# Kernel tuning notes

Hardware: AMD Instinct MI355X
Metric: run time of the kernel (lower is better)

Reference implementation:

```python
import jax, jax.numpy as jnp
import numpy as np

N, E, DIN, DH, DP = 100000, 1600000, 128, 128, 64
BN_EPS = 1e-5


def setup_inputs() -> dict:
    key = jax.random.key(0)
    ks = jax.random.split(key, 24)

    def lin(k, fan_in, shape):
        return jax.random.normal(k, shape, jnp.float32) / np.sqrt(fan_in)

    inp = {
        "x": jax.random.normal(ks[0], (N, DIN), jnp.float32),
        "edge_index": jax.random.randint(ks[1], (2, E), 0, N, dtype=jnp.int32),
        "edge_type": jax.random.randint(ks[2], (E,), 0, 2, dtype=jnp.int32),
        "edge_weight": jax.random.uniform(ks[3], (E,), jnp.float32),
        "seed_node_id": 12345,
        # feature transform
        "ft_w": lin(ks[4], DIN, (DIN, DH)),
        "ft_b": jnp.zeros((DH,), jnp.float32),
        # GCN block 0: 2 layers, stacked along axis 0
        "g0_w": lin(ks[5], DH, (2, DH, DH)),
        "g0_b": jnp.zeros((2, DH), jnp.float32),
        "g0_gamma": jnp.ones((2, DH), jnp.float32),
        "g0_beta": jnp.zeros((2, DH), jnp.float32),
        "g0_rm": 0.1 * jax.random.normal(ks[6], (2, DH), jnp.float32),
        "g0_rv": 0.5 + jax.random.uniform(ks[7], (2, DH), jnp.float32),
        # GCN block 1
        "g1_w": lin(ks[8], DH, (2, DH, DH)),
        "g1_b": jnp.zeros((2, DH), jnp.float32),
        "g1_gamma": jnp.ones((2, DH), jnp.float32),
        "g1_beta": jnp.zeros((2, DH), jnp.float32),
        "g1_rm": 0.1 * jax.random.normal(ks[9], (2, DH), jnp.float32),
        "g1_rv": 0.5 + jax.random.uniform(ks[10], (2, DH), jnp.float32),
        # predictor (input = 4*DH)
        "p_w1": lin(ks[11], 4 * DH, (4 * DH, DP)),
        "p_b1": jnp.zeros((DP,), jnp.float32),
        "p_w2": lin(ks[12], DP, (DP, DP)),
        "p_b2": jnp.zeros((DP,), jnp.float32),
        "p_w3": lin(ks[13], DP, (DP, 1)),
        "p_b3": jnp.zeros((1,), jnp.float32),
    }
    return inp


def _gcn_conv(x, src, dst, w_e, W, b):
    # PyG GCNConv: linear transform, add self-loops (weight 1), symmetric norm, scatter-add, bias.
    h = x @ W                                               # [N, DH]
    deg = jax.ops.segment_sum(w_e, dst, num_segments=N) + 1.0
    dis = jax.lax.rsqrt(deg)
    coef = dis[src] * w_e * dis[dst]                        # [E]
    agg = jax.ops.segment_sum(coef[:, None] * h[src], dst, num_segments=N)
    return agg + h * (1.0 / deg)[:, None] + b               # self-loop norm = 1/deg


def _bn_eval(o, gamma, beta, rm, rv):
    return (o - rm) * gamma * jax.lax.rsqrt(rv + BN_EPS) + beta


def _gcn_block(x, src, dst, w_e, W, b, gamma, beta, rm, rv):
    # layer 0: no residual, followed by ReLU (dropout is a no-op in eval)
    h = _bn_eval(_gcn_conv(x, src, dst, w_e, W[0], b[0]), gamma[0], beta[0], rm[0], rv[0])
    h = jax.nn.relu(h)
    # layer 1: residual (in == out)
    h2 = _bn_eval(_gcn_conv(h, src, dst, w_e, W[1], b[1]), gamma[1], beta[1], rm[1], rv[1])
    return h2 + h


def reference(x, edge_index, edge_type, edge_weight, seed_node_id,
              ft_w, ft_b,
              g0_w, g0_b, g0_gamma, g0_beta, g0_rm, g0_rv,
              g1_w, g1_b, g1_gamma, g1_beta, g1_rm, g1_rv,
              p_w1, p_b1, p_w2, p_b2, p_w3, p_b3):
    src, dst = edge_index[0], edge_index[1]
    h = jax.nn.relu(x @ ft_w + ft_b)
    # edge-type masking via zeroed weights (identical math to slicing the edge list)
    w0 = edge_weight * (edge_type == 0).astype(edge_weight.dtype)
    w1 = edge_weight * (edge_type == 1).astype(edge_weight.dtype)
    x0 = _gcn_block(h, src, dst, w0, g0_w, g0_b, g0_gamma, g0_beta, g0_rm, g0_rv)
    x1 = _gcn_block(h, src, dst, w1, g1_w, g1_b, g1_gamma, g1_beta, g1_rm, g1_rv)
    s0 = jnp.broadcast_to(x0[seed_node_id], (N, DH))
    s1 = jnp.broadcast_to(x1[seed_node_id], (N, DH))
    xc = jnp.concatenate([x0, x1, s0, s1], axis=1)          # [N, 4*DH]
    z = jax.nn.relu(xc @ p_w1 + p_b1)
    z = jax.nn.relu(z @ p_w2 + p_b2)
    out = z @ p_w3 + p_b3                                   # [N, 1]
    return out.squeeze(-1)                                  # [N]
```

## Files before the change

### kernel.cpp

```cpp
#include <hip/hip_runtime.h>
#include <hip/hip_bf16.h>
#include <stdint.h>

#define N_NODES 100000

typedef unsigned short us16;
typedef short bf16x8 __attribute__((ext_vector_type(8)));
typedef float f32x4 __attribute__((ext_vector_type(4)));

__device__ __forceinline__ float us2f(us16 u){
  union{ unsigned int i; float f; } x; x.i = ((unsigned int)u) << 16; return x.f;
}
__device__ __forceinline__ us16 f2us(float f){
  union{ float f; unsigned int i; } x; x.f = f;
  unsigned int i = x.i;
  unsigned int r = (i + 0x7FFFu + ((i >> 16) & 1u)) >> 16;
  return (us16)r;
}

__global__ __launch_bounds__(256) void k_init(int* __restrict__ cnt, int n2){
  int i = blockIdx.x*256 + threadIdx.x;
  if (i < n2) cnt[i]=0;
}

__global__ __launch_bounds__(256) void k_cnt(const int* __restrict__ dst,
                                             const int* __restrict__ et,
                                             int* __restrict__ cnt,
                                             int* __restrict__ eofs, int E){
  int e = blockIdx.x*256 + threadIdx.x;
  if (e>=E) return;
  int d = dst[e]; int t = et[e];
  eofs[e] = atomicAdd(&cnt[t*N_NODES + d], 1);
}

__global__ __launch_bounds__(256) void k_scan_reduce(const int* __restrict__ in, int* __restrict__ bsum, int M){
  __shared__ int sd[256];
  int base = blockIdx.x*2048; int t = threadIdx.x;
  int sum = 0;
  #pragma unroll
  for(int i=0;i<8;i++){ int p = base + t*8 + i; if(p<M) sum += in[p]; }
  sd[t]=sum; __syncthreads();
  for(int s=128;s>0;s>>=1){ if(t<s) sd[t]+=sd[t+s]; __syncthreads(); }
  if(t==0) bsum[blockIdx.x]=sd[0];
}
__global__ void k_scan_top(int* __restrict__ bsum, int B){
  if (threadIdx.x==0){ int run=0; for(int i=0;i<B;i++){ int v=bsum[i]; bsum[i]=run; run+=v; } }
}
__global__ __launch_bounds__(256) void k_scan_apply(const int* __restrict__ in, const int* __restrict__ bsum,
                                                    int* __restrict__ out, int M){
  __shared__ int sd[256];
  int base = blockIdx.x*2048; int t = threadIdx.x;
  int loc[8]; int sum=0;
  #pragma unroll
  for(int i=0;i<8;i++){ int p = base + t*8 + i; int v = (p<M)?in[p]:0; loc[i]=sum; sum+=v; }
  sd[t]=sum; __syncthreads();
  for(int ofs=1;ofs<256;ofs<<=1){
    int v = (t>=ofs)? sd[t-ofs] : 0;
    __syncthreads();
    sd[t]+=v;
    __syncthreads();
  }
  int excl = ((t==0)?0:sd[t-1]) + bsum[blockIdx.x];
  #pragma unroll
  for(int i=0;i<8;i++){ int p = base + t*8 + i; if(p<M) out[p]=excl+loc[i]; }
}

__global__ __launch_bounds__(256) void k_edge_fill(const int* __restrict__ src, const int* __restrict__ dst,
  const int* __restrict__ et, const float* __restrict__ ew,
  const int* __restrict__ rp, const int* __restrict__ eofs,
  uint2* __restrict__ csr, int E){
  int e = blockIdx.x*256+threadIdx.x;
  if(e>=E) return;
  int s=src[e], d=dst[e], t=et[e]; float w=ew[e];
  int idx = t*N_NODES + d;
  int pos = rp[idx] + eofs[e];
  csr[pos] = make_uint2((unsigned)s, __float_as_uint(w));
}

__global__ __launch_bounds__(256) void k_deg_csr(const uint2* __restrict__ csr,
                                                 const int* __restrict__ rp, const int* __restrict__ cnt,
                                                 float* __restrict__ disA, int M){
  int i = blockIdx.x*256+threadIdx.x;
  if(i>=M) return;
  int e0 = rp[i], c = cnt[i];
  float s = 1.0f;
  for(int e=e0; e<e0+c; e++) s += __uint_as_float(csr[e].y);
  disA[i] = rsqrtf(s);
}

__global__ __launch_bounds__(256) void k_prepw(const float* __restrict__ ft_w,
                                               const float* __restrict__ g0_w, const float* __restrict__ g1_w,
                                               const float* __restrict__ p_w1, const float* __restrict__ p_w2,
                                               us16* __restrict__ wt){
  int m = blockIdx.y;
  const float* srcp; int K, NCc; us16* dstp;
  switch(m){
    case 0: srcp=ft_w;        K=128; NCc=128; dstp=wt;        break;
    case 1: srcp=g0_w;        K=128; NCc=128; dstp=wt+16384;  break;
    case 2: srcp=g0_w+16384;  K=128; NCc=128; dstp=wt+32768;  break;
    case 3: srcp=g1_w;        K=128; NCc=128; dstp=wt+49152;  break;
    case 4: srcp=g1_w+16384;  K=128; NCc=128; dstp=wt+65536;  break;
    case 5: srcp=p_w1;        K=256; NCc=64;  dstp=wt+81920;  break;
    default:srcp=p_w2;        K=64;  NCc=64;  dstp=wt+98304;  break;
  }
  int idx = blockIdx.x*256+threadIdx.x;
  if(idx >= K*NCc) return;
  int nn = idx / K, k = idx - nn*K;
  dstp[idx] = f2us(srcp[(size_t)k*NCc + nn]);
}

template<int NC, typename AT>
__global__ __launch_bounds__(256) void k_mgemm(const AT* __restrict__ A0, const AT* __restrict__ A1,
                 int lda, const us16* __restrict__ Wt,
                 const float* __restrict__ bias, const float* __restrict__ addv,
                 const float* __restrict__ rowscale,
                 us16* __restrict__ C, int ldc, int n, int KC, int relu){
  constexpr int NB = NC/16;
  __shared__ us16 Alds[128*64];
  __shared__ us16 Wlds[NC*64];
  const int tid = threadIdx.x;
  const int lane = tid & 63, wid = tid >> 6;
  const int rowBase = blockIdx.x*128;
  f32x4 zero = {0.f,0.f,0.f,0.f};
  f32x4 acc[2][NB];
  #pragma unroll
  for(int m=0;m<2;m++)
    #pragma unroll
    for(int nb=0;nb<NB;nb++) acc[m][nb] = zero;

  for(int kk=0; kk<KC; kk+=64){
    const AT* Ab = (kk<128)? A0 : A1;
    const int kc = (kk<128)? kk : (kk-128);
    #pragma unroll
    for(int p=0;p<4;p++){
      int idx = p*256 + tid;
      int r = idx>>3, u = idx&7;
      int row = rowBase + r;
      uint4 v = make_uint4(0u,0u,0u,0u);
      if(row<n){
        if constexpr (sizeof(AT)==2){
          v = *(const uint4*)(Ab + (size_t)row*lda + kc + u*8);
        } else {
          float4 f0 = *(const float4*)(Ab + (size_t)row*lda + kc + u*8);
          float4 f1 = *(const float4*)(Ab + (size_t)row*lda + kc + u*8 + 4);
          us16 tmp[8] = {f2us(f0.x),f2us(f0.y),f2us(f0.z),f2us(f0.w),
                         f2us(f1.x),f2us(f1.y),f2us(f1.z),f2us(f1.w)};
          v = *(const uint4*)tmp;
        }
      }
      *(uint4*)&Alds[(r*8 + (u ^ (r&7)))*8] = v;
    }
    #pragma unroll
    for(int p=0;p<NB/2;p++){
      int idx = p*256 + tid;
      int cI = idx>>3, u = idx&7;
      uint4 v = *(const uint4*)(Wt + (size_t)cI*KC + kk + u*8);
      *(uint4*)&Wlds[(cI*8 + (u ^ (cI&7)))*8] = v;
    }
    __syncthreads();
    #pragma unroll
    for(int ks=0;ks<2;ks++){
      bf16x8 af[2];
      #pragma unroll
      for(int m=0;m<2;m++){
        int r = wid*32 + m*16 + (lane&15);
        int u = (ks*4 + (lane>>4)) ^ (r&7);
        af[m] = *(const bf16x8*)&Alds[(r*8+u)*8];
      }
      #pragma unroll
      for(int nb=0;nb<NB;nb++){
        int c2 = nb*16 + (lane&15);
        int u = (ks*4 + (lane>>4)) ^ (c2&7);
        bf16x8 bfv = *(const bf16x8*)&Wlds[(c2*8+u)*8];
        #pragma unroll
        for(int m=0;m<2;m++)
          acc[m][nb] = __builtin_amdgcn_mfma_f32_16x16x32_bf16(af[m], bfv, acc[m][nb], 0,0,0);
      }
    }
    __syncthreads();
  }
  float rs[2][4];
  #pragma unroll
  for(int m=0;m<2;m++)
    #pragma unroll
    for(int j=0;j<4;j++){
      int row = rowBase + wid*32 + m*16 + (lane>>4)*4 + j;
      rs[m][j] = (rowscale && row<n) ? rowscale[row] : 1.0f;
    }
  #pragma unroll
  for(int nb=0;nb<NB;nb++){
    int col = nb*16 + (lane&15);
    float badd = (bias? bias[col]:0.f) + (addv? addv[col]:0.f);
    #pragma unroll
    for(int m=0;m<2;m++){
      #pragma unroll
      for(int j=0;j<4;j++){
        int row = rowBase + wid*32 + m*16 + (lane>>4)*4 + j;
        if(row<n){
          float v = acc[m][nb][j]*rs[m][j] + badd;
          if(relu) v = fmaxf(v,0.f);
          C[(size_t)row*ldc + col] = f2us(v);
        }
      }
    }
  }
}

__global__ __launch_bounds__(256) void k_agg(const us16* __restrict__ T,
  const uint2* __restrict__ csr,
  const int* __restrict__ rp, const int* __restrict__ cnt, int rowOfs,
  const float* __restrict__ dis,
  const float* __restrict__ bias, const float* __restrict__ gamma, const float* __restrict__ beta,
  const float* __restrict__ rm, const float* __restrict__ rv,
  const us16* __restrict__ resid,
  us16* __restrict__ out, int relu, int n){
  const int wid = threadIdx.x >> 6, lane = threadIdx.x & 63;
  const int hw = lane >> 5;
  const int sl = lane & 31;
  int r = blockIdx.x*8 + wid*2 + hw;
  if (r >= n) return;
  const int c0 = sl*4;
  int idx = rowOfs + r;
  int e0 = rp[idx];
  int ec = cnt[idx];
  const uint2* cp = csr + e0;
  float a0=0.f, a1=0.f, a2=0.f, a3=0.f;
  int nchunk = ec >> 2;
  int rem = ec & 3;
  for(int ch=0; ch<nchunk; ch++){
    uint2 q0 = cp[0], q1 = cp[1], q2 = cp[2], q3 = cp[3];
    cp += 4;
    uint2 va = *(const uint2*)(T + (size_t)q0.x*128 + c0);
    uint2 vb = *(const uint2*)(T + (size_t)q1.x*128 + c0);
    uint2 vc = *(const uint2*)(T + (size_t)q2.x*128 + c0);
    uint2 vd = *(const uint2*)(T + (size_t)q3.x*128 + c0);
    float ca = __uint_as_float(q0.y), cb = __uint_as_float(q1.y);
    float cc = __uint_as_float(q2.y), cd = __uint_as_float(q3.y);
    a0 += ca*us2f((us16)(va.x & 0xffffu));
    a1 += ca*us2f((us16)(va.x >> 16));
    a2 += ca*us2f((us16)(va.y & 0xffffu));
    a3 += ca*us2f((us16)(va.y >> 16));
    a0 += cb*us2f((us16)(vb.x & 0xffffu));
    a1 += cb*us2f((us16)(vb.x >> 16));
    a2 += cb*us2f((us16)(vb.y & 0xffffu));
    a3 += cb*us2f((us16)(vb.y >> 16));
    a0 += cc*us2f((us16)(vc.x & 0xffffu));
    a1 += cc*us2f((us16)(vc.x >> 16));
    a2 += cc*us2f((us16)(vc.y & 0xffffu));
    a3 += cc*us2f((us16)(vc.y >> 16));
    a0 += cd*us2f((us16)(vd.x & 0xffffu));
    a1 += cd*us2f((us16)(vd.x >> 16));
    a2 += cd*us2f((us16)(vd.y & 0xffffu));
    a3 += cd*us2f((us16)(vd.y >> 16));
  }
  for(int i=0;i<rem;i++){
    uint2 q = cp[i];
    float c = __uint_as_float(q.y);
    uint2 v = *(const uint2*)(T + (size_t)q.x*128 + c0);
    a0 += c*us2f((us16)(v.x & 0xffffu));
    a1 += c*us2f((us16)(v.x >> 16));
    a2 += c*us2f((us16)(v.y & 0xffffu));
    a3 += c*us2f((us16)(v.y >> 16));
  }
  uint2 vs = *(const uint2*)(T + (size_t)r*128 + c0);
  a0 += us2f((us16)(vs.x & 0xffffu));
  a1 += us2f((us16)(vs.x >> 16));
  a2 += us2f((us16)(vs.y & 0xffffu));
  a3 += us2f((us16)(vs.y >> 16));
  float disr = dis[r];
  float4 bi = *(const float4*)(bias + c0);
  float4 ga = *(const float4*)(gamma + c0);
  float4 be = *(const float4*)(beta + c0);
  float4 rmv= *(const float4*)(rm + c0);
  float4 rvv= *(const float4*)(rv + c0);
  float o0 = a0*disr + bi.x;
  float o1 = a1*disr + bi.y;
  float o2 = a2*disr + bi.z;
  float o3 = a3*disr + bi.w;
  o0 = (o0 - rmv.x)*(ga.x*rsqrtf(rvv.x + 1e-5f)) + be.x;
  o1 = (o1 - rmv.y)*(ga.y*rsqrtf(rvv.y + 1e-5f)) + be.y;
  o2 = (o2 - rmv.z)*(ga.z*rsqrtf(rvv.z + 1e-5f)) + be.z;
  o3 = (o3 - rmv.w)*(ga.w*rsqrtf(rvv.w + 1e-5f)) + be.w;
  if (relu){
    o0=fmaxf(o0,0.f); o1=fmaxf(o1,0.f); o2=fmaxf(o2,0.f); o3=fmaxf(o3,0.f);
  }
  if (resid){
    uint2 vr = *(const uint2*)(resid + (size_t)r*128 + c0);
    o0 += us2f((us16)(vr.x & 0xffffu));
    o1 += us2f((us16)(vr.x >> 16));
    o2 += us2f((us16)(vr.y & 0xffffu));
    o3 += us2f((us16)(vr.y >> 16));
  }
  uint2 up;
  up.x = (unsigned)f2us(o0) | ((unsigned)f2us(o1) << 16);
  up.y = (unsigned)f2us(o2) | ((unsigned)f2us(o3) << 16);
  *(uint2*)(out + (size_t)r*128 + c0) = up;
}

__global__ void k_const64(const us16* __restrict__ X0, const us16* __restrict__ X1,
                          const int* __restrict__ seed,
                          const float* __restrict__ pw1, const float* __restrict__ pb1,
                          float* __restrict__ c64){
  int j = threadIdx.x;
  int s = seed[0];
  const us16* x0 = X0 + (size_t)s*128;
  const us16* x1 = X1 + (size_t)s*128;
  float acc = pb1[j];
  #pragma unroll 8
  for(int k=0;k<128;k++) acc += us2f(x0[k]) * pw1[(256+k)*64 + j];
  #pragma unroll 8
  for(int k=0;k<128;k++) acc += us2f(x1[k]) * pw1[(384+k)*64 + j];
  c64[j]=acc;
}

__global__ __launch_bounds__(256) void k_outdot(const us16* __restrict__ Z2, const float* __restrict__ w3,
                                                const float* __restrict__ b3, float* __restrict__ out, int n){
  int r = blockIdx.x*256 + threadIdx.x;
  if(r>=n) return;
  const us16* z = Z2 + (size_t)r*64;
  float acc = b3[0];
  #pragma unroll 8
  for(int j=0;j<64;j++) acc += us2f(z[j])*w3[j];
  out[r]=acc;
}

extern "C" void kernel_launch(void* const* d_in, const int* in_sizes, int n_in,
                              void* d_out, int out_size, void* d_ws, size_t ws_size,
                              hipStream_t stream){
  const int N = N_NODES;
  const int E = in_sizes[2];
  const float* x   = (const float*)d_in[0];
  const int*   ei  = (const int*)d_in[1];
  const int*   et  = (const int*)d_in[2];
  const float* ew  = (const float*)d_in[3];
  const int*   seed= (const int*)d_in[4];
  const float* ft_w= (const float*)d_in[5];
  const float* ft_b= (const float*)d_in[6];
  const float* g0_w= (const float*)d_in[7];
  const float* g0_b= (const float*)d_in[8];
  const float* g0_g= (const float*)d_in[9];
  const float* g0_be=(const float*)d_in[10];
  const float* g0_rm=(const float*)d_in[11];
  const float* g0_rv=(const float*)d_in[12];
  const float* g1_w= (const float*)d_in[13];
  const float* g1_b= (const float*)d_in[14];
  const float* g1_g= (const float*)d_in[15];
  const float* g1_be=(const float*)d_in[16];
  const float* g1_rm=(const float*)d_in[17];
  const float* g1_rv=(const float*)d_in[18];
  const float* p_w1= (const float*)d_in[19];
  const float* p_b1= (const float*)d_in[20];
  const float* p_w2= (const float*)d_in[21];
  const float* p_b2= (const float*)d_in[22];
  const float* p_w3= (const float*)d_in[23];
  const float* p_b3= (const float*)d_in[24];
  float* out = (float*)d_out;

  char* wsp = (char*)d_ws;
  auto alloc = [&](size_t bytes)->char*{ char* p = wsp; wsp += (bytes + 255) & ~(size_t)255; return p; };
  us16* B0 = (us16*)alloc((size_t)N*128*2);
  us16* B1 = (us16*)alloc((size_t)N*128*2);
  us16* B2 = (us16*)alloc((size_t)N*128*2);
  us16* B3 = (us16*)alloc((size_t)N*128*2);
  uint2* csr = (uint2*)alloc((size_t)E*8);
  float* disA=(float*)alloc((size_t)2*N*4);
  int* cnt =(int*)alloc((size_t)2*N*4);
  int* rp  =(int*)alloc((size_t)2*N*4);
  int* bsum=(int*)alloc(4096);
  float* c64=(float*)alloc(256);
  us16* wt =(us16*)alloc((size_t)102400*2);
  int* eofs = (int*)B0;
  us16* Z1 = B0;
  us16* Z2 = B1;

  const int* srcp = ei;
  const int* dstp = ei + E;

  int M = 2*N;
  k_init<<<(M+255)/256,256,0,stream>>>(cnt,M);
  k_cnt<<<(E+255)/256,256,0,stream>>>(dstp,et,cnt,eofs,E);
  int SB = (M+2047)/2048;
  k_scan_reduce<<<SB,256,0,stream>>>(cnt,bsum,M);
  k_scan_top<<<1,64,0,stream>>>(bsum,SB);
  k_scan_apply<<<SB,256,0,stream>>>(cnt,bsum,rp,M);
  k_edge_fill<<<(E+255)/256,256,0,stream>>>(srcp,dstp,et,ew,rp,eofs,csr,E);
  k_deg_csr<<<(M+255)/256,256,0,stream>>>(csr,rp,cnt,disA,M);

  dim3 pg(64,7);
  k_prepw<<<pg,256,0,stream>>>(ft_w,g0_w,g1_w,p_w1,p_w2,wt);

  const us16* wt_ft = wt;
  const us16* wt_g00= wt+16384;
  const us16* wt_g01= wt+32768;
  const us16* wt_g10= wt+49152;
  const us16* wt_g11= wt+65536;
  const us16* wt_p1 = wt+81920;
  const us16* wt_p2 = wt+98304;
  const float* dis0 = disA;
  const float* dis1 = disA + N;

  int GB = (N+127)/128;
  int AB = (N+7)/8;
  k_mgemm<128,float><<<GB,256,0,stream>>>(x,x,128, wt_ft, ft_b, nullptr, nullptr, B0,128, N,128,1);
  k_mgemm<128,us16><<<GB,256,0,stream>>>(B0,B0,128, wt_g00, nullptr,nullptr, dis0, B1,128, N,128,0);
  k_mgemm<128,us16><<<GB,256,0,stream>>>(B0,B0,128, wt_g10, nullptr,nullptr, dis1, B2,128, N,128,0);
  k_agg<<<AB,256,0,stream>>>(B1,csr,rp,cnt,0,dis0,
                             g0_b,g0_g,g0_be,g0_rm,g0_rv, nullptr, B0,1,N);
  k_mgemm<128,us16><<<GB,256,0,stream>>>(B0,B0,128, wt_g01, nullptr,nullptr, dis0, B1,128, N,128,0);
  k_agg<<<AB,256,0,stream>>>(B1,csr,rp,cnt,0,dis0,
                             g0_b+128,g0_g+128,g0_be+128,g0_rm+128,g0_rv+128, B0, B3,0,N);
  k_agg<<<AB,256,0,stream>>>(B2,csr,rp,cnt,N,dis1,
                             g1_b,g1_g,g1_be,g1_rm,g1_rv, nullptr, B0,1,N);
  k_mgemm<128,us16><<<GB,256,0,stream>>>(B0,B0,128, wt_g11, nullptr,nullptr, dis1, B1,128, N,128,0);
  k_agg<<<AB,256,0,stream>>>(B1,csr,rp,cnt,N,dis1,
                             g1_b+128,g1_g+128,g1_be+128,g1_rm+128,g1_rv+128, B0, B2,0,N);
  k_const64<<<1,64,0,stream>>>(B3,B2,seed,p_w1,p_b1,c64);
  k_mgemm<64,us16><<<GB,256,0,stream>>>(B3,B2,128, wt_p1, nullptr, c64, nullptr, Z1,64, N,256,1);
  k_mgemm<64,us16><<<GB,256,0,stream>>>(Z1,Z1,64,  wt_p2, p_b2, nullptr, nullptr, Z2,64, N,64,1);
  k_outdot<<<(N+255)/256,256,0,stream>>>(Z2,p_w3,p_b3,out,N);
}
```

Measured before the change: 445.0 us.

## Co-schedule graph CSR build with dense GEMMs via block-range dispatch kernels

The edge-count atomics now share one launch with the feature-transform GEMM, and the CSR fill shares one with both first-layer GCN GEMMs. Blocks choose their role from their block index, so the scatter-bound graph work and the compute-bound GEMM work can occupy the GPU together and the number of launches drops. The source-side normalisation is moved out of the GEMM row scaling into a new pass that folds dis[src] into the CSR edge weights, and the self-loop term now uses dis squared in the aggregation. The cost is an extra pass over the edges and larger shared-memory use in the fused kernels, which may lower occupancy for the graph-side blocks.

```diff
diff --git a/kernel.cpp b/kernel.cpp
--- a/kernel.cpp
+++ b/kernel.cpp
@@ -21,16 +21,6 @@
 __global__ __launch_bounds__(256) void k_init(int* __restrict__ cnt, int n2){
   int i = blockIdx.x*256 + threadIdx.x;
   if (i < n2) cnt[i]=0;
-}
-
-__global__ __launch_bounds__(256) void k_cnt(const int* __restrict__ dst,
-                                             const int* __restrict__ et,
-                                             int* __restrict__ cnt,
-                                             int* __restrict__ eofs, int E){
-  int e = blockIdx.x*256 + threadIdx.x;
-  if (e>=E) return;
-  int d = dst[e]; int t = et[e];
-  eofs[e] = atomicAdd(&cnt[t*N_NODES + d], 1);
 }
 
 __global__ __launch_bounds__(256) void k_scan_reduce(const int* __restrict__ in, int* __restrict__ bsum, int M){
@@ -65,18 +55,6 @@
   for(int i=0;i<8;i++){ int p = base + t*8 + i; if(p<M) out[p]=excl+loc[i]; }
 }
 
-__global__ __launch_bounds__(256) void k_edge_fill(const int* __restrict__ src, const int* __restrict__ dst,
-  const int* __restrict__ et, const float* __restrict__ ew,
-  const int* __restrict__ rp, const int* __restrict__ eofs,
-  uint2* __restrict__ csr, int E){
-  int e = blockIdx.x*256+threadIdx.x;
-  if(e>=E) return;
-  int s=src[e], d=dst[e], t=et[e]; float w=ew[e];
-  int idx = t*N_NODES + d;
-  int pos = rp[idx] + eofs[e];
-  csr[pos] = make_uint2((unsigned)s, __float_as_uint(w));
-}
-
 __global__ __launch_bounds__(256) void k_deg_csr(const uint2* __restrict__ csr,
                                                  const int* __restrict__ rp, const int* __restrict__ cnt,
                                                  float* __restrict__ disA, int M){
@@ -86,6 +64,18 @@
   float s = 1.0f;
   for(int e=e0; e<e0+c; e++) s += __uint_as_float(csr[e].y);
   disA[i] = rsqrtf(s);
+}
+
+__global__ __launch_bounds__(256) void k_coef(uint2* __restrict__ csr,
+                                              const int* __restrict__ rp,
+                                              const float* __restrict__ disA, int E){
+  int e = blockIdx.x*256+threadIdx.x;
+  if(e>=E) return;
+  int rpN = rp[N_NODES];
+  int t = (e >= rpN) ? 1 : 0;
+  uint2 q = csr[e];
+  float w = __uint_as_float(q.y) * disA[t*N_NODES + (int)q.x];
+  csr[e] = make_uint2(q.x, __float_as_uint(w));
 }
 
 __global__ __launch_bounds__(256) void k_prepw(const float* __restrict__ ft_w,
@@ -110,17 +100,16 @@
 }
 
 template<int NC, typename AT>
-__global__ __launch_bounds__(256) void k_mgemm(const AT* __restrict__ A0, const AT* __restrict__ A1,
+__device__ __forceinline__ void mgemm_body(int bid,
+                 const AT* __restrict__ A0, const AT* __restrict__ A1,
                  int lda, const us16* __restrict__ Wt,
                  const float* __restrict__ bias, const float* __restrict__ addv,
-                 const float* __restrict__ rowscale,
-                 us16* __restrict__ C, int ldc, int n, int KC, int relu){
+                 us16* __restrict__ C, int ldc, int n, int KC, int relu,
+                 us16* Alds, us16* Wlds){
   constexpr int NB = NC/16;
-  __shared__ us16 Alds[128*64];
-  __shared__ us16 Wlds[NC*64];
   const int tid = threadIdx.x;
   const int lane = tid & 63, wid = tid >> 6;
-  const int rowBase = blockIdx.x*128;
+  const int rowBase = bid*128;
   f32x4 zero = {0.f,0.f,0.f,0.f};
   f32x4 acc[2][NB];
   #pragma unroll
@@ -179,14 +168,6 @@
     }
     __syncthreads();
   }
-  float rs[2][4];
-  #pragma unroll
-  for(int m=0;m<2;m++)
-    #pragma unroll
-    for(int j=0;j<4;j++){
-      int row = rowBase + wid*32 + m*16 + (lane>>4)*4 + j;
-      rs[m][j] = (rowscale && row<n) ? rowscale[row] : 1.0f;
-    }
   #pragma unroll
   for(int nb=0;nb<NB;nb++){
     int col = nb*16 + (lane&15);
@@ -197,12 +178,66 @@
       for(int j=0;j<4;j++){
         int row = rowBase + wid*32 + m*16 + (lane>>4)*4 + j;
         if(row<n){
-          float v = acc[m][nb][j]*rs[m][j] + badd;
+          float v = acc[m][nb][j] + badd;
           if(relu) v = fmaxf(v,0.f);
           C[(size_t)row*ldc + col] = f2us(v);
         }
       }
     }
+  }
+}
+
+template<int NC, typename AT>
+__global__ __launch_bounds__(256) void k_mgemm(const AT* __restrict__ A0, const AT* __restrict__ A1,
+                 int lda, const us16* __restrict__ Wt,
+                 const float* __restrict__ bias, const float* __restrict__ addv,
+                 us16* __restrict__ C, int ldc, int n, int KC, int relu){
+  __shared__ us16 smem[128*64 + NC*64];
+  mgemm_body<NC,AT>(blockIdx.x, A0,A1,lda, Wt, bias,addv, C,ldc, n,KC,relu, smem, smem+128*64);
+}
+
+__global__ __launch_bounds__(256) void k_cnt_ft(const int* __restrict__ dst, const int* __restrict__ et,
+    int* __restrict__ cnt, int* __restrict__ eofs, int E, int CB,
+    const float* __restrict__ x, const us16* __restrict__ wt_ft, const float* __restrict__ ft_b,
+    us16* __restrict__ B0, int n){
+  __shared__ us16 smem[128*64 + 128*64];
+  int b = blockIdx.x;
+  if (b < CB){
+    int e = b*256 + threadIdx.x;
+    if (e < E){
+      int d = dst[e]; int t = et[e];
+      eofs[e] = atomicAdd(&cnt[t*N_NODES + d], 1);
+    }
+  } else {
+    mgemm_body<128,float>(b - CB, x, x, 128, wt_ft, ft_b, nullptr, B0, 128, n, 128, 1,
+                          smem, smem + 128*64);
+  }
+}
+
+__global__ __launch_bounds__(256) void k_fill_l0(
+    const int* __restrict__ src, const int* __restrict__ dst,
+    const int* __restrict__ et, const float* __restrict__ ew,
+    const int* __restrict__ rp, const int* __restrict__ eofs,
+    uint2* __restrict__ csr, int E, int FB, int GB,
+    const us16* __restrict__ B0,
+    const us16* __restrict__ wt_g00, const us16* __restrict__ wt_g10,
+    us16* __restrict__ B1, us16* __restrict__ B2, int n){
+  __shared__ us16 smem[128*64 + 128*64];
+  int b = blockIdx.x;
+  if (b < FB){
+    int e = b*256 + threadIdx.x;
+    if (e < E){
+      int s=src[e], d=dst[e], t=et[e]; float w=ew[e];
+      int idx = t*N_NODES + d;
+      int pos = rp[idx] + eofs[e];
+      csr[pos] = make_uint2((unsigned)s, __float_as_uint(w));
+    }
+  } else if (b < FB + GB){
+    mgemm_body<128,us16>(b - FB, B0, B0, 128, wt_g00, nullptr, nullptr, B1, 128, n, 128, 0,
+                         smem, smem + 128*64);
+  } else {
+    mgemm_body<128,us16>(b - FB - GB, B0, B0, 128, wt_g10, nullptr, nullptr, B2, 128, n, 128, 0,
+                         smem, smem + 128*64);
   }
 }
 
@@ -262,21 +297,17 @@
     a2 += c*us2f((us16)(v.y & 0xffffu));
     a3 += c*us2f((us16)(v.y >> 16));
   }
+  float disr = dis[r]; float invdeg = disr*disr;
   uint2 vs = *(const uint2*)(T + (size_t)r*128 + c0);
-  a0 += us2f((us16)(vs.x & 0xffffu));
-  a1 += us2f((us16)(vs.x >> 16));
-  a2 += us2f((us16)(vs.y & 0xffffu));
-  a3 += us2f((us16)(vs.y >> 16));
-  float disr = dis[r];
   float4 bi = *(const float4*)(bias + c0);
   float4 ga = *(const float4*)(gamma + c0);
   float4 be = *(const float4*)(beta + c0);
   float4 rmv= *(const float4*)(rm + c0);
   float4 rvv= *(const float4*)(rv + c0);
-  float o0 = a0*disr + bi.x;
-  float o1 = a1*disr + bi.y;
-  float o2 = a2*disr + bi.z;
-  float o3 = a3*disr + bi.w;
+  float o0 = a0*disr + us2f((us16)(vs.x & 0xffffu))*invdeg + bi.x;
+  float o1 = a1*disr + us2f((us16)(vs.x >> 16))*invdeg + bi.y;
+  float o2 = a2*disr + us2f((us16)(vs.y & 0xffffu))*invdeg + bi.z;
+  float o3 = a3*disr + us2f((us16)(vs.y >> 16))*invdeg + bi.w;
   o0 = (o0 - rmv.x)*(ga.x*rsqrtf(rvv.x + 1e-5f)) + be.x;
   o1 = (o1 - rmv.y)*(ga.y*rsqrtf(rvv.y + 1e-5f)) + be.y;
   o2 = (o2 - rmv.z)*(ga.z*rsqrtf(rvv.z + 1e-5f)) + be.z;
@@ -369,7 +400,7 @@
   int* bsum=(int*)alloc(4096);
   float* c64=(float*)alloc(256);
   us16* wt =(us16*)alloc((size_t)102400*2);
-  int* eofs = (int*)B0;
+  int* eofs = (int*)B3;
   us16* Z1 = B0;
   us16* Z2 = B1;
 
@@ -377,15 +408,12 @@
   const int* dstp = ei + E;
 
   int M = 2*N;
+  int CB = (E+255)/256;
+  int GB = (N+127)/128;
+  int AB = (N+7)/8;
+  int SB = (M+2047)/2048;
+
   k_init<<<(M+255)/256,256,0,stream>>>(cnt,M);
-  k_cnt<<<(E+255)/256,256,0,stream>>>(dstp,et,cnt,eofs,E);
-  int SB = (M+2047)/2048;
-  k_scan_reduce<<<SB,256,0,stream>>>(cnt,bsum,M);
-  k_scan_top<<<1,64,0,stream>>>(bsum,SB);
-  k_scan_apply<<<SB,256,0,stream>>>(cnt,bsum,rp,M);
-  k_edge_fill<<<(E+255)/256,256,0,stream>>>(srcp,dstp,et,ew,rp,eofs,csr,E);
-  k_deg_csr<<<(M+255)/256,256,0,stream>>>(csr,rp,cnt,disA,M);
-
   dim3 pg(64,7);
   k_prepw<<<pg,256,0,stream>>>(ft_w,g0_w,g1_w,p_w1,p_w2,wt);
 
@@ -399,23 +427,27 @@
   const float* dis0 = disA;
   const float* dis1 = disA + N;
 
-  int GB = (N+127)/128;
-  int AB = (N+7)/8;
-  k_mgemm<128,float><<<GB,256,0,stream>>>(x,x,128, wt_ft, ft_b, nullptr, nullptr, B0,128, N,128,1);
-  k_mgemm<128,us16><<<GB,256,0,stream>>>(B0,B0,128, wt_g00, nullptr,nullptr, dis0, B1,128, N,128,0);
-  k_mgemm<128,us16><<<GB,256,0,stream>>>(B0,B0,128, wt_g10, nullptr,nullptr, dis1, B2,128, N,128,0);
+  k_cnt_ft<<<CB+GB,256,0,stream>>>(dstp,et,cnt,eofs,E,CB, x,wt_ft,ft_b,B0,N);
+  k_scan_reduce<<<SB,256,0,stream>>>(cnt,bsum,M);
+  k_scan_top<<<1,64,0,stream>>>(bsum,SB);
+  k_scan_apply<<<SB,256,0,stream>>>(cnt,bsum,rp,M);
+  k_fill_l0<<<CB+2*GB,256,0,stream>>>(srcp,dstp,et,ew,rp,eofs,csr,E,CB,GB,
+                                      B0,wt_g00,wt_g10,B1,B2,N);
+  k_deg_csr<<<(M+255)/256,256,0,stream>>>(csr,rp,cnt,disA,M);
+  k_coef<<<(E+255)/256,256,0,stream>>>(csr,rp,disA,E);
+
   k_agg<<<AB,256,0,stream>>>(B1,csr,rp,cnt,0,dis0,
                              g0_b,g0_g,g0_be,g0_rm,g0_rv, nullptr, B0,1,N);
-  k_mgemm<128,us16><<<GB,256,0,stream>>>(B0,B0,128, wt_g01, nullptr,nullptr, dis0, B1,128, N,128,0);
+  k_mgemm<128,us16><<<GB,256,0,stream>>>(B0,B0,128, wt_g01, nullptr,nullptr, B1,128, N,128,0);
   k_agg<<<AB,256,0,stream>>>(B1,csr,rp,cnt,0,dis0,
                              g0_b+128,g0_g+128,g0_be+128,g0_rm+128,g0_rv+128, B0, B3,0,N);
   k_agg<<<AB,256,0,stream>>>(B2,csr,rp,cnt,N,dis1,
                              g1_b,g1_g,g1_be,g1_rm,g1_rv, nullptr, B0,1,N);
-  k_mgemm<128,us16><<<GB,256,0,stream>>>(B0,B0,128, wt_g11, nullptr,nullptr, dis1, B1,128, N,128,0);
+  k_mgemm<128,us16><<<GB,256,0,stream>>>(B0,B0,128, wt_g11, nullptr,nullptr, B1,128, N,128,0);
   k_agg<<<AB,256,0,stream>>>(B1,csr,rp,cnt,N,dis1,
                              g1_b+128,g1_g+128,g1_be+128,g1_rm+128,g1_rv+128, B0, B2,0,N);
   k_const64<<<1,64,0,stream>>>(B3,B2,seed,p_w1,p_b1,c64);
-  k_mgemm<64,us16><<<GB,256,0,stream>>>(B3,B2,128, wt_p1, nullptr, c64, nullptr, Z1,64, N,256,1);
-  k_mgemm<64,us16><<<GB,256,0,stream>>>(Z1,Z1,64,  wt_p2, p_b2, nullptr, nullptr, Z2,64, N,64,1);
+  k_mgemm<64,us16><<<GB,256,0,stream>>>(B3,B2,128, wt_p1, nullptr, c64, Z1,64, N,256,1);
+  k_mgemm<64,us16><<<GB,256,0,stream>>>(Z1,Z1,64,  wt_p2, p_b2, nullptr, Z2,64, N,64,1);
   k_outdot<<<(N+255)/256,256,0,stream>>>(Z2,p_w3,p_b3,out,N);
 }
```

Result: no change. 437.5 us (-1.7%).
